# Optimization experiments

Hardware: AMD Instinct MI355X
Metric: run time of the kernel (lower is better)

## Reference

```python
import jax, jax.numpy as jnp
import numpy as np
from jax import lax

VDECAY, VTH, GRAD_WIN, GRAD_AMP = 0.5, 0.5, 0.5, 1.0

@jax.custom_vjp
def spike(v):
    return (v > VTH).astype(v.dtype)

def _spike_fwd(v):
    return spike(v), v

def _spike_bwd(v, g):
    # rectangular surrogate gradient
    win = (jnp.abs(v - VTH) <= GRAD_WIN).astype(g.dtype)
    return (GRAD_AMP * g * win,)

spike.defvjp(_spike_fwd, _spike_bwd)

def setup_inputs() -> dict:
    key = jax.random.key(0)
    ks = jax.random.split(key, 3)
    B, D_IN, T, H, D_OUT = 256, 700, 250, 1024, 20
    spike_data = (jax.random.uniform(ks[0], (B, D_IN, T)) < 0.1).astype(jnp.float32)
    W_hid = jax.random.normal(ks[1], (H, D_IN), dtype=jnp.float32) * (1.0 / np.sqrt(D_IN))
    W_out = jax.random.normal(ks[2], (D_OUT, H), dtype=jnp.float32) * (1.0 / np.sqrt(H))
    return {
        "spike_data": spike_data,
        "W_hid": W_hid,
        "W_out": W_out,
        "hid_spike0": jnp.zeros((B, H), jnp.float32),
        "hid_volt0": jnp.zeros((B, H), jnp.float32),
        "out_spike0": jnp.zeros((B, D_OUT), jnp.float32),
        "out_volt0": jnp.zeros((B, D_OUT), jnp.float32),
        "batch_size": 256,
        "spike_ts": 250,
    }

def reference(spike_data, W_hid, W_out, hid_spike0, hid_volt0, out_spike0, out_volt0, batch_size, spike_ts):
    # [B, D_in, T] -> [T, B, D_in] for scan over time
    xs = jnp.moveaxis(spike_data.reshape(batch_size, -1, spike_ts), -1, 0)

    def step(carry, s_in):
        hs, hv, os_, ov = carry
        hv = hv * VDECAY * (1.0 - hs) + s_in @ W_hid.T      # leaky integrate, reset on spike
        hs = spike(hv)                                       # hidden spikes
        ov = ov * VDECAY * (1.0 - os_) + hs @ W_out.T
        os_ = spike(ov)
        return (hs, hv, os_, ov), os_

    _, out_spikes = lax.scan(step, (hid_spike0, hid_volt0, out_spike0, out_volt0), xs)
    return jnp.sum(out_spikes, axis=0)  # [B, D_out] spike counts
```

## Files before the change

### kernel.cpp

```cpp
#include <hip/hip_runtime.h>
#include <stdint.h>

#define B      256
#define DIN    700
#define T      250
#define H      1024
#define DOUT   20
#define NW_IN  11
#define NW_INP 12
#define NW_H   16
#define LMAX   160
#define JSENT  44896

typedef unsigned long long u64;

__global__ void prep_weights(const float* __restrict__ W_hid,
                             const float* __restrict__ W_out,
                             float* __restrict__ Wt,
                             float* __restrict__ WoT) {
    int idx = blockIdx.x * 256 + threadIdx.x;
    if (blockIdx.x < 2800) {
        int d = idx / H;
        int h = idx - d * H;
        Wt[idx] = W_hid[h * DIN + d];
    } else {
        int i = idx - 2800 * 256;
        int h = i / DOUT;
        int o = i - h * DOUT;
        WoT[i] = W_out[o * H + h];
    }
}

__global__ void prep_bits(const float* __restrict__ spk,
                          u64* __restrict__ bits) {
    int b  = blockIdx.x >> 2;
    int wc = blockIdx.x & 3;
    int t  = threadIdx.x;
    if (t >= T) return;
    int w0 = wc * 3;
    int w1 = (wc == 3) ? NW_IN : w0 + 3;
    const float* base = spk + (size_t)b * DIN * T + t;
    for (int w = w0; w < w1; ++w) {
        u64 m = 0;
#pragma unroll
        for (int j = 0; j < 64; ++j) {
            int d = (w << 6) + j;
            if (d < DIN) {
                float x = base[(size_t)d * T];
                m |= (u64)(x > 0.5f) << j;
            }
        }
        bits[((size_t)b * T + t) * NW_INP + w] = m;
    }
}

__global__ void __launch_bounds__(256)
prep_lists2(const u64* __restrict__ bits,
            unsigned short* __restrict__ lists,
            unsigned short* __restrict__ nrow) {
    __shared__ unsigned short scr[4][LMAX];

    int wv   = threadIdx.x >> 6;
    int lane = threadIdx.x & 63;
    int row  = blockIdx.x * 4 + wv;

    const u64* wp = bits + (size_t)row * NW_INP;
    u64 mw = (lane < NW_IN) ? wp[lane] : 0ull;

    for (int i = lane; i < LMAX; i += 64) scr[wv][i] = (unsigned short)JSENT;

    u64 lowmask = (1ull << lane) - 1ull;

    int baseA = 0;
#pragma unroll
    for (int k = 0; k < 6; ++k) {
        u64 m = __shfl(mw, k);
        if (k == 5) m &= (1ull << 30) - 1ull;
        if ((m >> lane) & 1ull) {
            int pos = baseA + __popcll(m & lowmask);
            int j = (k << 6) + lane;
            if (pos < LMAX)
                scr[wv][pos] = (unsigned short)(j * 128 + ((j & 7) << 4));
        }
        baseA += __popcll(m);
    }
    int cA = (baseA + 7) >> 3;
    int bs = cA * 8;

    int baseB = 0;
#pragma unroll
    for (int k = 5; k < NW_IN; ++k) {
        u64 m = __shfl(mw, k);
        if (k == 5) m &= ~((1ull << 30) - 1ull);
        if ((m >> lane) & 1ull) {
            int pos = bs + baseB + __popcll(m & lowmask);
            int jl = (k << 6) + lane - 350;
            if (pos < LMAX)
                scr[wv][pos] = (unsigned short)(jl * 128 + ((jl & 7) << 4));
        }
        baseB += __popcll(m);
    }
    int cB = (baseB + 7) >> 3;

    if (lane == 0) nrow[row] = (unsigned short)(cA | (cB << 8));

    __syncthreads();

    const unsigned* s32 = (const unsigned*)scr[wv];
    unsigned* g32 = (unsigned*)(lists + (size_t)row * LMAX);
    g32[lane] = s32[lane];
    if (lane < 16) g32[64 + lane] = s32[64 + lane];
}

__global__ void __launch_bounds__(256)
sort_rows(const unsigned short* __restrict__ nrow,
          unsigned char* __restrict__ permA,
          unsigned char* __restrict__ permB) {
    __shared__ unsigned cntA[24], cntB[24], offA[24], offB[24];
    int b = blockIdx.x, tid = threadIdx.x;
    if (tid < 24) { cntA[tid] = 0; cntB[tid] = 0; }
    __syncthreads();
    int cA = 0, cB = 0;
    if (tid < T) {
        unsigned cc = nrow[b * T + tid];
        cA = cc & 0xff;          if (cA > 23) cA = 23;
        cB = (cc >> 8) & 0xff;   if (cB > 23) cB = 23;
        atomicAdd(&cntA[cA], 1);
        atomicAdd(&cntB[cB], 1);
    }
    __syncthreads();
    if (tid == 0) { unsigned s = 0; for (int i = 0; i < 24; ++i) { offA[i] = s; s += cntA[i]; cntA[i] = 0; } }
    if (tid == 1) { unsigned s = 0; for (int i = 0; i < 24; ++i) { offB[i] = s; s += cntB[i]; cntB[i] = 0; } }
    __syncthreads();
    if (tid < T) {
        unsigned pA = offA[cA] + atomicAdd(&cntA[cA], 1);
        unsigned pB = offB[cB] + atomicAdd(&cntB[cB], 1);
        permA[b * 256 + pA] = (unsigned char)tid;
        permB[b * 256 + pB] = (unsigned char)tid;
    }
}

__global__ void __launch_bounds__(512, 2)
hidden_slice2(const unsigned short* __restrict__ lists,
              const unsigned short* __restrict__ nrow,
              const unsigned char* __restrict__ permA,
              const unsigned char* __restrict__ permB,
              const float* __restrict__ Wt,
              const float* __restrict__ hs0,
              const float* __restrict__ hv0,
              u64* __restrict__ hsbits) {
    __shared__ float wlds[351 * 32];
    __shared__ float cur[250 * 32];

    int s    = blockIdx.x;
    int b    = blockIdx.y;
    int tid  = threadIdx.x;
    int wv   = tid >> 6;
    int lane = tid & 63;
    int g    = lane >> 3;
    int li   = lane & 7;
    int lxor = li << 4;

    for (int p = 0; p < 2; ++p) {
        {
            int jr  = tid >> 3;
            int lis = tid & 7;
#pragma unroll
            for (int base_j = 0; base_j < 384; base_j += 64) {
                int j = base_j + jr;
                if (j < 351) {
                    float4 v;
                    if (j < 350)
                        v = *(const float4*)(Wt + (size_t)(p * 350 + j) * H + s * 32 + lis * 4);
                    else
                        v = make_float4(0.0f, 0.0f, 0.0f, 0.0f);
                    *(float4*)((char*)wlds + j * 128 + ((lis ^ (j & 7)) << 4)) = v;
                }
            }
        }
        __syncthreads();

        const unsigned char* pm = (p ? permB : permA) + b * 256;

        for (int sweep = 0; sweep < 4; ++sweep) {
            int rr = sweep * 64 + wv * 8 + g;
            if (rr < 250) {
                int r   = pm[rr];
                int row = b * T + r;
                unsigned cc = nrow[row];
                int cA = cc & 0xff;
                int c  = p ? ((cc >> 8) & 0xff) : cA;
                const uint4* qp = (const uint4*)(lists + (size_t)row * LMAX + (p ? cA * 8 : 0));

                float a0, a1, a2, a3;
                if (p == 0) {
                    a0 = a1 = a2 = a3 = 0.0f;
                } else {
                    float4 cv = *(const float4*)((char*)cur + r * 128 + lxor);
                    a0 = cv.x; a1 = cv.y; a2 = cv.z; a3 = cv.w;
                }

                if (c > 0) {
                    uint4 w4 = qp[0];
                    int ch = 0;
                    for (;;) {
                        uint4 nw = (ch + 1 < c) ? qp[ch + 1] : w4;
                        int e0 = w4.x & 0xffff, e1 = w4.x >> 16;
                        int e2 = w4.y & 0xffff, e3 = w4.y >> 16;
                        int e4 = w4.z & 0xffff, e5 = w4.z >> 16;
                        int e6 = w4.w & 0xffff, e7 = w4.w >> 16;
                        float4 v0 = *(const float4*)((char*)wlds + (e0 ^ lxor));
                        float4 v1 = *(const float4*)((char*)wlds + (e1 ^ lxor));
                        float4 v2 = *(const float4*)((char*)wlds + (e2 ^ lxor));
                        float4 v3 = *(const float4*)((char*)wlds + (e3 ^ lxor));
                        float4 v4 = *(const float4*)((char*)wlds + (e4 ^ lxor));
                        float4 v5 = *(const float4*)((char*)wlds + (e5 ^ lxor));
                        float4 v6 = *(const float4*)((char*)wlds + (e6 ^ lxor));
                        float4 v7 = *(const float4*)((char*)wlds + (e7 ^ lxor));
                        a0 += v0.x; a1 += v0.y; a2 += v0.z; a3 += v0.w;
                        a0 += v1.x; a1 += v1.y; a2 += v1.z; a3 += v1.w;
                        a0 += v2.x; a1 += v2.y; a2 += v2.z; a3 += v2.w;
                        a0 += v3.x; a1 += v3.y; a2 += v3.z; a3 += v3.w;
                        a0 += v4.x; a1 += v4.y; a2 += v4.z; a3 += v4.w;
                        a0 += v5.x; a1 += v5.y; a2 += v5.z; a3 += v5.w;
                        a0 += v6.x; a1 += v6.y; a2 += v6.z; a3 += v6.w;
                        a0 += v7.x; a1 += v7.y; a2 += v7.z; a3 += v7.w;
                        ++ch;
                        if (ch >= c) break;
                        w4 = nw;
                    }
                }
                float4 o; o.x = a0; o.y = a1; o.z = a2; o.w = a3;
                *(float4*)((char*)cur + r * 128 + lxor) = o;
            }
        }
        __syncthreads();
    }

    if (wv == 0) {
        int l = lane & 31;
        int h = s * 32 + l;
        float keep = hv0[b * H + h] * 0.5f * (1.0f - hs0[b * H + h]);
        unsigned* hp = (unsigned*)hsbits;
        float c = cur[l];
        for (int t = 0; t < T; ++t) {
            float cn = (t + 1 < T) ? cur[(t + 1) * 32 + l] : 0.0f;
            float hv = keep + c;
            bool sp = hv > 0.5f;
            keep = sp ? 0.0f : hv * 0.5f;
            u64 ball = __ballot(sp);
            if (lane == 0)
                hp[(size_t)(b * T + t) * 32 + s] = (unsigned)ball;
            c = cn;
        }
    }
}

__global__ void __launch_bounds__(1024)
hidden_fused(const u64* __restrict__ bits,
             const float* __restrict__ Wt,
             const float* __restrict__ hs0,
             const float* __restrict__ hv0,
             u64* __restrict__ hsbits) {
    __shared__ int idx_l[2][256];

    int b = blockIdx.x;
    int h = threadIdx.x;
    int wv   = h >> 6;
    int lane = h & 63;

    float keep = hv0[b * H + h] * 0.5f * (1.0f - hs0[b * H + h]);

    const u64* bb = bits + (size_t)b * T * NW_INP;

    for (int t = 0; t < T; ++t) {
        const u64* wp = bb + (size_t)t * NW_INP;
        u64 w[NW_IN];
#pragma unroll
        for (int k = 0; k < NW_IN; ++k) w[k] = wp[k];

        int base[NW_IN + 1];
        base[0] = 0;
#pragma unroll
        for (int k = 0; k < NW_IN; ++k) base[k + 1] = base[k] + __popcll(w[k]);
        int n = base[NW_IN];

        int buf = t & 1;
        if (wv < NW_IN) {
            u64 m = w[wv];
            if ((m >> lane) & 1ull) {
                int pos = base[wv] + __popcll(m & ((1ull << lane) - 1ull));
                idx_l[buf][pos] = (wv << 6) + lane;
            }
        }
        __syncthreads();

        const int* il = idx_l[buf];
        float cur2 = 0.0f;
        int i = 0;
        for (; i + 8 <= n; i += 8) {
            int j0 = il[i + 0], j1 = il[i + 1], j2 = il[i + 2], j3 = il[i + 3];
            int j4 = il[i + 4], j5 = il[i + 5], j6 = il[i + 6], j7 = il[i + 7];
            float v0 = Wt[(size_t)j0 * H + h];
            float v1 = Wt[(size_t)j1 * H + h];
            float v2 = Wt[(size_t)j2 * H + h];
            float v3 = Wt[(size_t)j3 * H + h];
            float v4 = Wt[(size_t)j4 * H + h];
            float v5 = Wt[(size_t)j5 * H + h];
            float v6 = Wt[(size_t)j6 * H + h];
            float v7 = Wt[(size_t)j7 * H + h];
            cur2 += v0; cur2 += v1; cur2 += v2; cur2 += v3;
            cur2 += v4; cur2 += v5; cur2 += v6; cur2 += v7;
        }
        for (; i < n; ++i) cur2 += Wt[(size_t)il[i] * H + h];

        float hv = keep + cur2;
        bool sp = hv > 0.5f;
        keep = sp ? 0.0f : hv * 0.5f;
        u64 ball = __ballot(sp);
        if (lane == 0)
            hsbits[((size_t)b * T + t) * NW_H + wv] = ball;
    }
}

__global__ void __launch_bounds__(256)
out_currents(const u64* __restrict__ hsbits,
             const float* __restrict__ WoT,
             float* __restrict__ Iout) {
    __shared__ int lidx[4][2][256];

    int wv   = threadIdx.x >> 6;
    int lane = threadIdx.x & 63;
    int row  = blockIdx.x * 4 + wv;

    const u64* wp = hsbits + (size_t)row * NW_H;

    float acc = 0.0f;
#pragma unroll
    for (int g = 0; g < 4; ++g) {
        u64 w[4];
#pragma unroll
        for (int k = 0; k < 4; ++k) w[k] = wp[g * 4 + k];

        int base[5];
        base[0] = 0;
#pragma unroll
        for (int k = 0; k < 4; ++k) base[k + 1] = base[k] + __popcll(w[k]);
        int n = base[4];

        int buf = g & 1;
#pragma unroll
        for (int k = 0; k < 4; ++k) {
            u64 m = w[k];
            if ((m >> lane) & 1ull) {
                int pos = base[k] + __popcll(m & ((1ull << lane) - 1ull));
                lidx[wv][buf][pos] = ((g * 4 + k) << 6) + lane;
            }
        }
        __syncthreads();

        const int* il = lidx[wv][buf];
        int i = 0;
        for (; i + 4 <= n; i += 4) {
            int j0 = il[i + 0], j1 = il[i + 1], j2 = il[i + 2], j3 = il[i + 3];
            if (lane < DOUT) {
                float v0 = WoT[(size_t)j0 * DOUT + lane];
                float v1 = WoT[(size_t)j1 * DOUT + lane];
                float v2 = WoT[(size_t)j2 * DOUT + lane];
                float v3 = WoT[(size_t)j3 * DOUT + lane];
                acc += v0; acc += v1; acc += v2; acc += v3;
            }
        }
        for (; i < n; ++i) {
            if (lane < DOUT) acc += WoT[(size_t)il[i] * DOUT + lane];
        }
    }
    if (lane < DOUT) Iout[(size_t)row * DOUT + lane] = acc;
}

__global__ void __launch_bounds__(256)
out_scan(const float* __restrict__ Iout,
         const float* __restrict__ os0,
         const float* __restrict__ ov0,
         float* __restrict__ outp) {
    __shared__ float pan[T * DOUT];

    int b   = blockIdx.x;
    int tid = threadIdx.x;

    const float* src = Iout + (size_t)b * T * DOUT;
#pragma unroll
    for (int k = 0; k < 20; ++k) {
        int i = k * 256 + tid;
        if (i < T * DOUT) pan[i] = src[i];
    }
    __syncthreads();

    if (tid < DOUT) {
        int o = tid;
        int idx = b * DOUT + o;
        float ov = ov0[idx];
        float os = os0[idx];
        float keep = ov * 0.5f * (1.0f - os);
        float cnt = 0.0f;
#pragma unroll 5
        for (int t = 0; t < T; ++t) {
            float v = keep + pan[t * DOUT + o];
            float sp = (v > 0.5f) ? 1.0f : 0.0f;
            cnt += sp;
            keep = v * 0.5f * (1.0f - sp);
        }
        outp[idx] = cnt;
    }
}

extern "C" void kernel_launch(void* const* d_in, const int* in_sizes, int n_in,
                              void* d_out, int out_size, void* d_ws, size_t ws_size,
                              hipStream_t stream) {
    const float* spike = (const float*)d_in[0];
    const float* W_hid = (const float*)d_in[1];
    const float* W_out = (const float*)d_in[2];
    const float* hs0   = (const float*)d_in[3];
    const float* hv0   = (const float*)d_in[4];
    const float* os0   = (const float*)d_in[5];
    const float* ov0   = (const float*)d_in[6];
    float* outp = (float*)d_out;

    char* ws = (char*)d_ws;
    float*          Wt     = (float*)(ws);
    float*          WoT    = (float*)(ws + 2867200);
    u64*            bits   = (u64*)  (ws + 2949120);
    u64*            hsbits = (u64*)  (ws + 9093120);
    float*          Iout   = (float*)(ws + 17285120);
    unsigned short* lists  = (unsigned short*)(ws + 22405120);
    unsigned short* nrow   = (unsigned short*)(ws + 42885120);
    unsigned char*  permA  = (unsigned char*)(ws + 43013120);
    unsigned char*  permB  = (unsigned char*)(ws + 43078656);
    const size_t need = 43144192;

    prep_weights<<<2880, 256, 0, stream>>>(W_hid, W_out, Wt, WoT);
    prep_bits<<<1024, 256, 0, stream>>>(spike, bits);

    if (ws_size >= need) {
        prep_lists2<<<16000, 256, 0, stream>>>(bits, lists, nrow);
        sort_rows<<<B, 256, 0, stream>>>(nrow, permA, permB);
        hidden_slice2<<<dim3(32, 256), 512, 0, stream>>>(lists, nrow, permA, permB, Wt, hs0, hv0, hsbits);
    } else {
        hidden_fused<<<B, 1024, 0, stream>>>(bits, Wt, hs0, hv0, hsbits);
    }

    out_currents<<<16000, 256, 0, stream>>>(hsbits, WoT, Iout);
    out_scan<<<B, 256, 0, stream>>>(Iout, os0, ov0, outp);
}
```

Baseline: 994.8 us.

## Split hidden-current kernel into four input chunks and two time halves for occupancy

The sparse input index lists are now partitioned into four chunks of 175 inputs, padded to groups of 4 instead of 8. The hidden kernel processes time in two halves of 125 steps, which shrinks shared memory (weights 176x32, currents 125x32) so launch bounds can request 8 blocks per multiprocessor instead of 2. Rows are sorted per chunk and per time half to balance wave work. The costs are more weight reloads (8 passes instead of 2), more block barriers and smaller unrolled inner loops.

```diff
diff --git a/kernel.cpp b/kernel.cpp
--- a/kernel.cpp
+++ b/kernel.cpp
@@ -10,7 +10,7 @@
 #define NW_INP 12
 #define NW_H   16
 #define LMAX   160
-#define JSENT  44896
+#define JSENT2 22512
 
 typedef unsigned long long u64;
 
@@ -57,7 +57,7 @@
 __global__ void __launch_bounds__(256)
 prep_lists2(const u64* __restrict__ bits,
             unsigned short* __restrict__ lists,
-            unsigned short* __restrict__ nrow) {
+            unsigned* __restrict__ nrow) {
     __shared__ unsigned short scr[4][LMAX];
 
     int wv   = threadIdx.x >> 6;
@@ -67,43 +67,36 @@
     const u64* wp = bits + (size_t)row * NW_INP;
     u64 mw = (lane < NW_IN) ? wp[lane] : 0ull;
 
-    for (int i = lane; i < LMAX; i += 64) scr[wv][i] = (unsigned short)JSENT;
+    for (int i = lane; i < LMAX; i += 64) scr[wv][i] = (unsigned short)JSENT2;
 
     u64 lowmask = (1ull << lane) - 1ull;
-
-    int baseA = 0;
-#pragma unroll
-    for (int k = 0; k < 6; ++k) {
-        u64 m = __shfl(mw, k);
-        if (k == 5) m &= (1ull << 30) - 1ull;
-        if ((m >> lane) & 1ull) {
-            int pos = baseA + __popcll(m & lowmask);
-            int j = (k << 6) + lane;
-            if (pos < LMAX)
-                scr[wv][pos] = (unsigned short)(j * 128 + ((j & 7) << 4));
-        }
-        baseA += __popcll(m);
-    }
-    int cA = (baseA + 7) >> 3;
-    int bs = cA * 8;
-
-    int baseB = 0;
-#pragma unroll
-    for (int k = 5; k < NW_IN; ++k) {
-        u64 m = __shfl(mw, k);
-        if (k == 5) m &= ~((1ull << 30) - 1ull);
-        if ((m >> lane) & 1ull) {
-            int pos = bs + baseB + __popcll(m & lowmask);
-            int jl = (k << 6) + lane - 350;
-            if (pos < LMAX)
-                scr[wv][pos] = (unsigned short)(jl * 128 + ((jl & 7) << 4));
-        }
-        baseB += __popcll(m);
-    }
-    int cB = (baseB + 7) >> 3;
-
-    if (lane == 0) nrow[row] = (unsigned short)(cA | (cB << 8));
-
+    int pos = 0;
+    unsigned counts = 0;
+
+#pragma unroll
+    for (int p = 0; p < 4; ++p) {
+        int jlo = 175 * p, jhi = jlo + 175;
+        int n = 0;
+        for (int k = jlo >> 6; k <= (jhi - 1) >> 6; ++k) {
+            u64 m = __shfl(mw, k);
+            int lo = jlo - (k << 6);
+            int hi = jhi - (k << 6);
+            if (lo > 0)  m &= ~((1ull << lo) - 1ull);
+            if (hi < 64) m &= (1ull << hi) - 1ull;
+            if ((m >> lane) & 1ull) {
+                int q = pos + n + __popcll(m & lowmask);
+                int jl = (k << 6) + lane - jlo;
+                if (q < LMAX)
+                    scr[wv][q] = (unsigned short)(jl * 128 + ((jl & 7) << 4));
+            }
+            n += __popcll(m);
+        }
+        int c = (n + 3) >> 2;
+        counts |= (unsigned)c << (8 * p);
+        pos += c * 4;
+    }
+
+    if (lane == 0) nrow[row] = counts;
     __syncthreads();
 
     const unsigned* s32 = (const unsigned*)scr[wv];
@@ -113,44 +106,51 @@
 }
 
 __global__ void __launch_bounds__(256)
-sort_rows(const unsigned short* __restrict__ nrow,
-          unsigned char* __restrict__ permA,
-          unsigned char* __restrict__ permB) {
-    __shared__ unsigned cntA[24], cntB[24], offA[24], offB[24];
+sort_rows(const unsigned* __restrict__ nrow,
+          unsigned char* __restrict__ perm) {
+    __shared__ int cnt[8][32];
+    __shared__ int off[8][32];
     int b = blockIdx.x, tid = threadIdx.x;
-    if (tid < 24) { cntA[tid] = 0; cntB[tid] = 0; }
+    cnt[tid >> 5][tid & 31] = 0;
     __syncthreads();
-    int cA = 0, cB = 0;
+    unsigned cc = 0; int half = 0, lt = 0;
     if (tid < T) {
-        unsigned cc = nrow[b * T + tid];
-        cA = cc & 0xff;          if (cA > 23) cA = 23;
-        cB = (cc >> 8) & 0xff;   if (cB > 23) cB = 23;
-        atomicAdd(&cntA[cA], 1);
-        atomicAdd(&cntB[cB], 1);
+        cc = nrow[b * T + tid];
+        half = tid >= 125;
+        lt = tid - half * 125;
+#pragma unroll
+        for (int p = 0; p < 4; ++p) {
+            int c = (cc >> (8 * p)) & 0xff; if (c > 31) c = 31;
+            atomicAdd(&cnt[p * 2 + half][c], 1);
+        }
     }
     __syncthreads();
-    if (tid == 0) { unsigned s = 0; for (int i = 0; i < 24; ++i) { offA[i] = s; s += cntA[i]; cntA[i] = 0; } }
-    if (tid == 1) { unsigned s = 0; for (int i = 0; i < 24; ++i) { offB[i] = s; s += cntB[i]; cntB[i] = 0; } }
+    if (tid < 8) {
+        int s = 0;
+        for (int i = 0; i < 32; ++i) { off[tid][i] = s; s += cnt[tid][i]; cnt[tid][i] = 0; }
+    }
     __syncthreads();
     if (tid < T) {
-        unsigned pA = offA[cA] + atomicAdd(&cntA[cA], 1);
-        unsigned pB = offB[cB] + atomicAdd(&cntB[cB], 1);
-        permA[b * 256 + pA] = (unsigned char)tid;
-        permB[b * 256 + pB] = (unsigned char)tid;
-    }
-}
-
-__global__ void __launch_bounds__(512, 2)
-hidden_slice2(const unsigned short* __restrict__ lists,
-              const unsigned short* __restrict__ nrow,
-              const unsigned char* __restrict__ permA,
-              const unsigned char* __restrict__ permB,
+#pragma unroll
+        for (int p = 0; p < 4; ++p) {
+            int c = (cc >> (8 * p)) & 0xff; if (c > 31) c = 31;
+            int sidx = p * 2 + half;
+            int rank = off[sidx][c] + atomicAdd(&cnt[sidx][c], 1);
+            perm[((size_t)b * 8 + sidx) * 128 + rank] = (unsigned char)lt;
+        }
+    }
+}
+
+__global__ void __launch_bounds__(512, 8)
+hidden_slice3(const unsigned short* __restrict__ lists,
+              const unsigned* __restrict__ nrow,
+              const unsigned char* __restrict__ perm,
               const float* __restrict__ Wt,
               const float* __restrict__ hs0,
               const float* __restrict__ hv0,
               u64* __restrict__ hsbits) {
-    __shared__ float wlds[351 * 32];
-    __shared__ float cur[250 * 32];
+    __shared__ float wlds[176 * 32];
+    __shared__ float cur[125 * 32];
 
     int s    = blockIdx.x;
     int b    = blockIdx.y;
@@ -160,99 +160,100 @@
     int g    = lane >> 3;
     int li   = lane & 7;
     int lxor = li << 4;
-
-    for (int p = 0; p < 2; ++p) {
-        {
-            int jr  = tid >> 3;
-            int lis = tid & 7;
-#pragma unroll
-            for (int base_j = 0; base_j < 384; base_j += 64) {
-                int j = base_j + jr;
-                if (j < 351) {
-                    float4 v;
-                    if (j < 350)
-                        v = *(const float4*)(Wt + (size_t)(p * 350 + j) * H + s * 32 + lis * 4);
-                    else
-                        v = make_float4(0.0f, 0.0f, 0.0f, 0.0f);
-                    *(float4*)((char*)wlds + j * 128 + ((lis ^ (j & 7)) << 4)) = v;
-                }
-            }
-        }
-        __syncthreads();
-
-        const unsigned char* pm = (p ? permB : permA) + b * 256;
-
-        for (int sweep = 0; sweep < 4; ++sweep) {
-            int rr = sweep * 64 + wv * 8 + g;
-            if (rr < 250) {
-                int r   = pm[rr];
-                int row = b * T + r;
-                unsigned cc = nrow[row];
-                int cA = cc & 0xff;
-                int c  = p ? ((cc >> 8) & 0xff) : cA;
-                const uint4* qp = (const uint4*)(lists + (size_t)row * LMAX + (p ? cA * 8 : 0));
-
-                float a0, a1, a2, a3;
-                if (p == 0) {
-                    a0 = a1 = a2 = a3 = 0.0f;
-                } else {
-                    float4 cv = *(const float4*)((char*)cur + r * 128 + lxor);
-                    a0 = cv.x; a1 = cv.y; a2 = cv.z; a3 = cv.w;
-                }
-
-                if (c > 0) {
-                    uint4 w4 = qp[0];
-                    int ch = 0;
-                    for (;;) {
-                        uint4 nw = (ch + 1 < c) ? qp[ch + 1] : w4;
-                        int e0 = w4.x & 0xffff, e1 = w4.x >> 16;
-                        int e2 = w4.y & 0xffff, e3 = w4.y >> 16;
-                        int e4 = w4.z & 0xffff, e5 = w4.z >> 16;
-                        int e6 = w4.w & 0xffff, e7 = w4.w >> 16;
-                        float4 v0 = *(const float4*)((char*)wlds + (e0 ^ lxor));
-                        float4 v1 = *(const float4*)((char*)wlds + (e1 ^ lxor));
-                        float4 v2 = *(const float4*)((char*)wlds + (e2 ^ lxor));
-                        float4 v3 = *(const float4*)((char*)wlds + (e3 ^ lxor));
-                        float4 v4 = *(const float4*)((char*)wlds + (e4 ^ lxor));
-                        float4 v5 = *(const float4*)((char*)wlds + (e5 ^ lxor));
-                        float4 v6 = *(const float4*)((char*)wlds + (e6 ^ lxor));
-                        float4 v7 = *(const float4*)((char*)wlds + (e7 ^ lxor));
-                        a0 += v0.x; a1 += v0.y; a2 += v0.z; a3 += v0.w;
-                        a0 += v1.x; a1 += v1.y; a2 += v1.z; a3 += v1.w;
-                        a0 += v2.x; a1 += v2.y; a2 += v2.z; a3 += v2.w;
-                        a0 += v3.x; a1 += v3.y; a2 += v3.z; a3 += v3.w;
-                        a0 += v4.x; a1 += v4.y; a2 += v4.z; a3 += v4.w;
-                        a0 += v5.x; a1 += v5.y; a2 += v5.z; a3 += v5.w;
-                        a0 += v6.x; a1 += v6.y; a2 += v6.z; a3 += v6.w;
-                        a0 += v7.x; a1 += v7.y; a2 += v7.z; a3 += v7.w;
-                        ++ch;
-                        if (ch >= c) break;
-                        w4 = nw;
+    int l    = lane & 31;
+
+    float keep = 0.0f;
+    if (wv == 0) {
+        int h = s * 32 + l;
+        keep = hv0[b * H + h] * 0.5f * (1.0f - hs0[b * H + h]);
+    }
+    unsigned* hp = (unsigned*)hsbits;
+
+    for (int th = 0; th < 2; ++th) {
+        for (int p = 0; p < 4; ++p) {
+            {
+                int jr  = tid >> 3;
+                int lis = tid & 7;
+#pragma unroll
+                for (int bj = 0; bj < 192; bj += 64) {
+                    int jl = bj + jr;
+                    if (jl < 176) {
+                        float4 v = make_float4(0.0f, 0.0f, 0.0f, 0.0f);
+                        if (jl < 175)
+                            v = *(const float4*)(Wt + (size_t)(p * 175 + jl) * H + s * 32 + lis * 4);
+                        *(float4*)((char*)wlds + jl * 128 + ((lis ^ (jl & 7)) << 4)) = v;
                     }
                 }
-                float4 o; o.x = a0; o.y = a1; o.z = a2; o.w = a3;
-                *(float4*)((char*)cur + r * 128 + lxor) = o;
+            }
+            __syncthreads();
+
+            const unsigned char* pm = perm + ((size_t)b * 8 + p * 2 + th) * 128;
+
+#pragma unroll
+            for (int sweep = 0; sweep < 2; ++sweep) {
+                int rr = sweep * 64 + wv * 8 + g;
+                if (rr < 125) {
+                    int lr  = pm[rr];
+                    int r   = th * 125 + lr;
+                    int row = b * T + r;
+                    unsigned cc = nrow[row];
+                    int c = (cc >> (8 * p)) & 0xff;
+                    int offc = 0;
+                    if (p > 0) offc += (cc & 0xff);
+                    if (p > 1) offc += ((cc >> 8) & 0xff);
+                    if (p > 2) offc += ((cc >> 16) & 0xff);
+                    const uint2* qp = (const uint2*)(lists + (size_t)row * LMAX + offc * 4);
+                    char* cp = (char*)cur + lr * 128 + ((li ^ (lr & 7)) << 4);
+
+                    float a0, a1, a2, a3;
+                    if (p == 0) {
+                        a0 = a1 = a2 = a3 = 0.0f;
+                    } else {
+                        float4 cv = *(const float4*)cp;
+                        a0 = cv.x; a1 = cv.y; a2 = cv.z; a3 = cv.w;
+                    }
+
+                    if (c > 0) {
+                        uint2 w2 = qp[0];
+                        int ch = 0;
+                        for (;;) {
+                            uint2 nw = (ch + 1 < c) ? qp[ch + 1] : w2;
+                            int e0 = w2.x & 0xffff, e1 = w2.x >> 16;
+                            int e2 = w2.y & 0xffff, e3 = w2.y >> 16;
+                            float4 v0 = *(const float4*)((char*)wlds + (e0 ^ lxor));
+                            float4 v1 = *(const float4*)((char*)wlds + (e1 ^ lxor));
+                            float4 v2 = *(const float4*)((char*)wlds + (e2 ^ lxor));
+                            float4 v3 = *(const float4*)((char*)wlds + (e3 ^ lxor));
+                            a0 += v0.x; a1 += v0.y; a2 += v0.z; a3 += v0.w;
+                            a0 += v1.x; a1 += v1.y; a2 += v1.z; a3 += v1.w;
+                            a0 += v2.x; a1 += v2.y; a2 += v2.z; a3 += v2.w;
+                            a0 += v3.x; a1 += v3.y; a2 += v3.z; a3 += v3.w;
+                            ++ch;
+                            if (ch >= c) break;
+                            w2 = nw;
+                        }
+                    }
+                    float4 o; o.x = a0; o.y = a1; o.z = a2; o.w = a3;
+                    *(float4*)cp = o;
+                }
+            }
+            __syncthreads();
+        }
+
+        if (wv == 0) {
+            for (int lt = 0; lt < 125; ++lt) {
+                float cv = *(const float*)((char*)cur + lt * 128 +
+                                           (((l >> 2) ^ (lt & 7)) << 4) + (l & 3) * 4);
+                float hv = keep + cv;
+                bool sp = hv > 0.5f;
+                keep = sp ? 0.0f : hv * 0.5f;
+                u64 ball = __ballot(sp);
+                int t = th * 125 + lt;
+                if (lane == 0)
+                    hp[(size_t)(b * T + t) * 32 + s] = (unsigned)ball;
             }
         }
         __syncthreads();
-    }
-
-    if (wv == 0) {
-        int l = lane & 31;
-        int h = s * 32 + l;
-        float keep = hv0[b * H + h] * 0.5f * (1.0f - hs0[b * H + h]);
-        unsigned* hp = (unsigned*)hsbits;
-        float c = cur[l];
-        for (int t = 0; t < T; ++t) {
-            float cn = (t + 1 < T) ? cur[(t + 1) * 32 + l] : 0.0f;
-            float hv = keep + c;
-            bool sp = hv > 0.5f;
-            keep = sp ? 0.0f : hv * 0.5f;
-            u64 ball = __ballot(sp);
-            if (lane == 0)
-                hp[(size_t)(b * T + t) * 32 + s] = (unsigned)ball;
-            c = cn;
-        }
     }
 }
 
@@ -433,18 +434,17 @@
     u64*            hsbits = (u64*)  (ws + 9093120);
     float*          Iout   = (float*)(ws + 17285120);
     unsigned short* lists  = (unsigned short*)(ws + 22405120);
-    unsigned short* nrow   = (unsigned short*)(ws + 42885120);
-    unsigned char*  permA  = (unsigned char*)(ws + 43013120);
-    unsigned char*  permB  = (unsigned char*)(ws + 43078656);
-    const size_t need = 43144192;
+    unsigned*       nrow   = (unsigned*)(ws + 42885120);
+    unsigned char*  perm   = (unsigned char*)(ws + 43141120);
+    const size_t need = 43403264;
 
     prep_weights<<<2880, 256, 0, stream>>>(W_hid, W_out, Wt, WoT);
     prep_bits<<<1024, 256, 0, stream>>>(spike, bits);
 
     if (ws_size >= need) {
         prep_lists2<<<16000, 256, 0, stream>>>(bits, lists, nrow);
-        sort_rows<<<B, 256, 0, stream>>>(nrow, permA, permB);
-        hidden_slice2<<<dim3(32, 256), 512, 0, stream>>>(lists, nrow, permA, permB, Wt, hs0, hv0, hsbits);
+        sort_rows<<<B, 256, 0, stream>>>(nrow, perm);
+        hidden_slice3<<<dim3(32, 256), 512, 0, stream>>>(lists, nrow, perm, Wt, hs0, hv0, hsbits);
     } else {
         hidden_fused<<<B, 1024, 0, stream>>>(bits, Wt, hs0, hv0, hsbits);
     }
```

Result: no change. 988.0 us (-0.7%).
